# Kernel tuning notes

Measured on AMD Instinct MI355X. Metric: run time of the kernel, lower is better.

Reference implementation:

```python
import jax, jax.numpy as jnp
import numpy as np

N = 50000      # nodes
E = 800000     # edges (avg degree 16)
IN = 16        # input feature dim
H = 512        # hidden dim
L = 3          # num conv layers
G = 256        # graphs per batch
EPS = 1e-5


def setup_inputs() -> dict:
    key = jax.random.key(0)
    ks = jax.random.split(key, 10)
    s = lambda d: 1.0 / np.sqrt(d)
    x = jax.random.normal(ks[0], (N, IN), jnp.float32)
    edge_index = jax.random.randint(ks[1], (2, E), 0, N, dtype=jnp.int64)
    batch = jnp.sort(jax.random.randint(ks[2], (N,), 0, G, dtype=jnp.int64))
    W_in = jax.random.normal(ks[3], (IN, H), jnp.float32) * s(IN)
    b_in = jnp.zeros((H,), jnp.float32)
    W_root = jax.random.normal(ks[4], (L, H, H), jnp.float32) * s(H)
    W_neigh = jax.random.normal(ks[5], (L, H, H), jnp.float32) * s(H)
    b_conv = jnp.zeros((L, H), jnp.float32)
    ln_gamma = jnp.ones((L, H), jnp.float32)
    ln_beta = jnp.zeros((L, H), jnp.float32)
    W_out = jax.random.normal(ks[6], (H, H), jnp.float32) * s(H)
    b_out = jnp.zeros((H,), jnp.float32)
    return {
        'x': x, 'edge_index': edge_index, 'batch': batch,
        'W_in': W_in, 'b_in': b_in,
        'W_root': W_root, 'W_neigh': W_neigh, 'b_conv': b_conv,
        'ln_gamma': ln_gamma, 'ln_beta': ln_beta,
        'W_out': W_out, 'b_out': b_out,
    }


def layer_norm(h, gamma, beta):
    mu = jnp.mean(h, axis=-1, keepdims=True)
    var = jnp.mean((h - mu) ** 2, axis=-1, keepdims=True)
    return (h - mu) * jax.lax.rsqrt(var + EPS) * gamma + beta


def reference(x, edge_index, batch, W_in, b_in, W_root, W_neigh, b_conv,
              ln_gamma, ln_beta, W_out, b_out):
    src, dst = edge_index[0], edge_index[1]
    h = x @ W_in + b_in                                  # [N, H]
    for l in range(L):
        # GraphConv: root transform + sum-aggregated neighbor transform
        agg = jax.ops.segment_sum(h[src], dst, num_segments=N)   # [N, H]
        h = h @ W_root[l] + agg @ W_neigh[l] + b_conv[l]
        h = jax.nn.relu(layer_norm(h, ln_gamma[l], ln_beta[l]))
        # dropout is identity in eval mode
    # mean pool per graph
    pooled = jax.ops.segment_sum(h, batch, num_segments=G)        # [G, H]
    counts = jax.ops.segment_sum(jnp.ones((N, 1), h.dtype), batch, num_segments=G)
    pooled = pooled / jnp.maximum(counts, 1.0)
    return pooled @ W_out + b_out
```

## Files before the change

### kernel.cpp

```cpp
#include <hip/hip_runtime.h>
#include <hip/hip_fp16.h>
#include <stdint.h>

#define N_NODES 50000
#define N_EDGES 800000
#define DIM_IN  16
#define H       512
#define GRAPHS  256
#define AK      1024
#define KT_STEPS 32

typedef __attribute__((ext_vector_type(8))) short short8;
typedef __attribute__((ext_vector_type(8))) _Float16 half8;
typedef __attribute__((ext_vector_type(4))) float f32x4;
typedef __attribute__((ext_vector_type(2))) float f32x2;
typedef __attribute__((ext_vector_type(4))) unsigned int u32x4;
typedef __attribute__((ext_vector_type(2))) unsigned int u32x2;

__device__ __forceinline__ unsigned short f2bf(float f) {
    unsigned int u = __float_as_uint(f);
    return (unsigned short)((u + 0x7fffu + ((u >> 16) & 1u)) >> 16);
}
__device__ __forceinline__ unsigned short f2h(float f) {
    __half h = __float2half(f);
    return *(unsigned short*)&h;
}

#define GLOAD_LDS16(g, l) __builtin_amdgcn_global_load_lds( \
    (const __attribute__((address_space(1))) void*)(g), \
    (__attribute__((address_space(3))) void*)(l), 16, 0, 0)

__global__ void k_count(const int* __restrict__ ei, int* __restrict__ deg) {
    int t = blockIdx.x * 256 + threadIdx.x;
    if (t < N_EDGES) atomicAdd(&deg[ei[N_EDGES + t]], 1);
}

__global__ void k_scan1(const int* __restrict__ deg, int* __restrict__ off, int* __restrict__ bsum) {
    __shared__ int ls[512];
    int t = threadIdx.x; int gi = blockIdx.x * 512 + t;
    ls[t] = (gi < N_NODES) ? deg[gi] : 0;
    __syncthreads();
    for (int o = 1; o < 512; o <<= 1) {
        int u = (t >= o) ? ls[t - o] : 0;
        __syncthreads();
        ls[t] += u;
        __syncthreads();
    }
    if (gi < N_NODES) off[gi] = (t == 0) ? 0 : ls[t - 1];
    if (t == 511) bsum[blockIdx.x] = ls[511];
}

__global__ void k_scan2(int* bsum) {
    __shared__ int ls[128];
    int t = threadIdx.x;
    ls[t] = (t < 98) ? bsum[t] : 0;
    __syncthreads();
    for (int o = 1; o < 128; o <<= 1) {
        int u = (t >= o) ? ls[t - o] : 0;
        __syncthreads();
        ls[t] += u;
        __syncthreads();
    }
    if (t < 98) bsum[t] = (t == 0) ? 0 : ls[t - 1];
}

__global__ void k_scan3(int* __restrict__ off, const int* __restrict__ bsum, int* __restrict__ cur) {
    int i = blockIdx.x * 256 + threadIdx.x;
    if (i < N_NODES) {
        int v = off[i] + bsum[i >> 9];
        off[i] = v; cur[i] = v;
    }
    if (i == 0) off[N_NODES] = N_EDGES;
}

__global__ void k_fill(const int* __restrict__ ei, int* __restrict__ cur, int* __restrict__ csr) {
    int t = blockIdx.x * 256 + threadIdx.x;
    if (t < N_EDGES) {
        int d = ei[N_EDGES + t];
        int p = atomicAdd(&cur[d], 1);
        csr[p] = ei[t];
    }
}

__global__ void k_gemm_in(const float* __restrict__ x, const float* __restrict__ Win,
                          const float* __restrict__ bin, unsigned short* A,
                          unsigned char* __restrict__ h8) {
    __shared__ float Wl[DIM_IN * H];
    __shared__ float xl[16 * DIM_IN];
    __shared__ float bl[H];
    int t = threadIdx.x;
    const float4* W4 = (const float4*)Win;
    float4* Wl4 = (float4*)Wl;
#pragma unroll
    for (int i = 0; i < 8; i++) Wl4[t + 256 * i] = W4[t + 256 * i];
    bl[t] = bin[t]; bl[t + 256] = bin[t + 256];
    int r0 = blockIdx.x * 16;
    {
        int r = t >> 4, k = t & 15;
        int row = r0 + r;
        xl[t] = (row < N_NODES) ? x[row * DIM_IN + k] : 0.f;
    }
    __syncthreads();
    int c0 = t * 2;
    for (int r = 0; r < 16; r++) {
        int row = r0 + r;
        if (row >= N_NODES) break;
        float a0 = bl[c0], a1 = bl[c0 + 1];
#pragma unroll
        for (int k = 0; k < 16; k++) {
            float xv = xl[r * 16 + k];
            a0 += xv * Wl[k * 512 + c0];
            a1 += xv * Wl[k * 512 + c0 + 1];
        }
        unsigned int pack = ((unsigned int)f2bf(a1) << 16) | (unsigned int)f2bf(a0);
        *(unsigned int*)&A[(size_t)row * AK + c0] = pack;
        unsigned int pk8 = (unsigned int)__builtin_amdgcn_cvt_pk_fp8_f32(a0, a1, 0, false);
        *(unsigned short*)&h8[(size_t)row * 512 + c0] = (unsigned short)(pk8 & 0xffffu);
    }
}

__global__ void k_aggregate(const int* __restrict__ off, const int* __restrict__ csr,
                            const unsigned char* __restrict__ h8, unsigned short* A) {
    int w = threadIdx.x >> 6, lane = threadIdx.x & 63;
    int n = blockIdx.x * 4 + w;
    if (n >= N_NODES) return;
    int s = off[n], e = off[n + 1];
    float acc[8] = {0, 0, 0, 0, 0, 0, 0, 0};
    const unsigned char* Ab = h8 + (size_t)lane * 8;

#define ACC_FP8(vv) { \
    f32x2 p0 = __builtin_amdgcn_cvt_pk_f32_fp8((int)(vv)[0], false); \
    f32x2 p1 = __builtin_amdgcn_cvt_pk_f32_fp8((int)(vv)[0], true);  \
    f32x2 p2 = __builtin_amdgcn_cvt_pk_f32_fp8((int)(vv)[1], false); \
    f32x2 p3 = __builtin_amdgcn_cvt_pk_f32_fp8((int)(vv)[1], true);  \
    acc[0] += p0[0]; acc[1] += p0[1]; acc[2] += p1[0]; acc[3] += p1[1]; \
    acc[4] += p2[0]; acc[5] += p2[1]; acc[6] += p3[0]; acc[7] += p3[1]; }

    for (int base = s; base < e; base += 64) {
        int m = e - base; if (m > 64) m = 64;
        int idx = (lane < m) ? csr[base + lane] : 0;
        int g = 0;
        for (; g + 4 <= m; g += 4) {
            int sn0 = __shfl(idx, g);
            int sn1 = __shfl(idx, g + 1);
            int sn2 = __shfl(idx, g + 2);
            int sn3 = __shfl(idx, g + 3);
            u32x2 v0 = *(const u32x2*)(Ab + ((size_t)sn0 << 9));
            u32x2 v1 = *(const u32x2*)(Ab + ((size_t)sn1 << 9));
            u32x2 v2 = *(const u32x2*)(Ab + ((size_t)sn2 << 9));
            u32x2 v3 = *(const u32x2*)(Ab + ((size_t)sn3 << 9));
            ACC_FP8(v0); ACC_FP8(v1); ACC_FP8(v2); ACC_FP8(v3);
        }
        for (; g < m; g++) {
            int sn = __shfl(idx, g);
            u32x2 v = *(const u32x2*)(Ab + ((size_t)sn << 9));
            ACC_FP8(v);
        }
    }
#undef ACC_FP8
    u32x4 hv;
#pragma unroll
    for (int j = 0; j < 4; j++) {
        hv[j] = ((unsigned int)f2h(acc[2 * j + 1]) << 16) | (unsigned int)f2h(acc[2 * j]);
    }
    *(u32x4*)&A[(size_t)n * AK + 512 + lane * 8] = hv;
}

__global__ __launch_bounds__(512, 4)
void k_gemm_layer(unsigned short* A, const unsigned short* __restrict__ Bp,
                  const float* __restrict__ bias, const float* __restrict__ gamma,
                  const float* __restrict__ beta,
                  unsigned char* __restrict__ h8, int w8) {
    extern __shared__ __align__(16) char smem[];
    int t = threadIdx.x, w = t >> 6, lane = t & 63;
    int wr = w >> 1, wc = w & 1;
    int rblk = blockIdx.x * 64;

    f32x4 acc[16];
#pragma unroll
    for (int i = 0; i < 16; i++) acc[i] = (f32x4)(0.f);

    int rowSt = rblk + w * 16 + (lane & 15);
    if (rowSt >= N_NODES) rowSt = N_NODES - 1;
    const unsigned short* gAst = A + (size_t)rowSt * AK + (lane >> 4) * 8;
    const unsigned short* gB = Bp + (size_t)lane * 8;

    auto STAGE = [&](int kt, int buf) {
        char* base = smem + buf * 36864;
        const unsigned short* gBk = gB + (size_t)kt * 32 * 512;
#pragma unroll
        for (int i = 0; i < 4; i++) {
            int cf = w * 4 + i;
            GLOAD_LDS16(gBk + (size_t)cf * 512, base + cf * 1024);
        }
        if (w < 4) GLOAD_LDS16(gAst + kt * 32, base + 32768 + w * 1024);
    };

    STAGE(0, 0);
    __syncthreads();

    for (int kt = 0; kt < 16; kt++) {
        int cur = kt & 1;
        STAGE(kt + 1, cur ^ 1);
        char* base = smem + cur * 36864;
        short8 av = *(const short8*)(base + 32768 + wr * 1024 + lane * 16);
#pragma unroll
        for (int i = 0; i < 16; i++) {
            short8 bv = *(const short8*)(base + (wc * 16 + i) * 1024 + lane * 16);
            acc[i] = __builtin_amdgcn_mfma_f32_16x16x32_bf16(av, bv, acc[i], 0, 0, 0);
        }
        __syncthreads();
    }
    for (int kt = 16; kt < 32; kt++) {
        int cur = kt & 1;
        if (kt + 1 < 32) STAGE(kt + 1, cur ^ 1);
        char* base = smem + cur * 36864;
        half8 av = *(const half8*)(base + 32768 + wr * 1024 + lane * 16);
#pragma unroll
        for (int i = 0; i < 16; i++) {
            half8 bv = *(const half8*)(base + (wc * 16 + i) * 1024 + lane * 16);
            acc[i] = __builtin_amdgcn_mfma_f32_16x16x32_f16(av, bv, acc[i], 0, 0, 0);
        }
        __syncthreads();
    }

    int g = lane >> 4, cl = lane & 15;
    float s[4] = {0, 0, 0, 0}, q[4] = {0, 0, 0, 0};
#pragma unroll
    for (int i = 0; i < 16; i++) {
        int col = wc * 256 + i * 16 + cl;
        float b = bias[col];
        f32x4 a = acc[i];
#pragma unroll
        for (int r = 0; r < 4; r++) {
            float v = a[r] + b;
            a[r] = v;
            s[r] += v;
            q[r] += v * v;
        }
        acc[i] = a;
    }
#pragma unroll
    for (int m = 1; m < 16; m <<= 1) {
#pragma unroll
        for (int r = 0; r < 4; r++) {
            s[r] += __shfl_xor(s[r], m);
            q[r] += __shfl_xor(q[r], m);
        }
    }
    float* pbuf = (float*)smem;
    if (cl == 0) {
#pragma unroll
        for (int r = 0; r < 4; r++) {
            pbuf[((wr * 2 + wc) * 16) + g * 4 + r] = s[r];
            pbuf[256 + ((wr * 2 + wc) * 16) + g * 4 + r] = q[r];
        }
    }
    __syncthreads();
    float mean[4], rs[4];
#pragma unroll
    for (int r = 0; r < 4; r++) {
        float sf = pbuf[(wr * 2) * 16 + g * 4 + r] + pbuf[(wr * 2 + 1) * 16 + g * 4 + r];
        float qf = pbuf[256 + (wr * 2) * 16 + g * 4 + r] + pbuf[256 + (wr * 2 + 1) * 16 + g * 4 + r];
        mean[r] = sf * (1.f / 512.f);
        float var = qf * (1.f / 512.f) - mean[r] * mean[r];
        rs[r] = rsqrtf(var + 1e-5f);
    }
    int row0 = rblk + wr * 16 + g * 4;
    bool ok[4];
#pragma unroll
    for (int r = 0; r < 4; r++) ok[r] = (row0 + r) < N_NODES;
#pragma unroll
    for (int i = 0; i < 16; i++) {
        int col = wc * 256 + i * 16 + cl;
        float ga = gamma[col], be = beta[col];
        f32x4 a = acc[i];
#pragma unroll
        for (int r = 0; r < 4; r++) {
            float o = (a[r] - mean[r]) * rs[r] * ga + be;
            o = fmaxf(o, 0.f);
            if (ok[r]) {
                A[(size_t)(row0 + r) * AK + col] = f2bf(o);
                if (w8) {
                    unsigned int pk8 = (unsigned int)__builtin_amdgcn_cvt_pk_fp8_f32(o, o, 0, false);
                    h8[(size_t)(row0 + r) * 512 + col] = (unsigned char)(pk8 & 0xffu);
                }
            }
        }
    }
}

__global__ void k_pool(const unsigned short* __restrict__ A, const int* __restrict__ batch,
                       float* __restrict__ pooled) {
    __shared__ float part[4 * 512];
    __shared__ int se[2];
    int g = blockIdx.x, t = threadIdx.x, w = t >> 6, lane = t & 63;
    if (t == 0) {
        int lo = 0, hi = N_NODES;
        while (lo < hi) { int m = (lo + hi) >> 1; if (batch[m] < g) lo = m + 1; else hi = m; }
        se[0] = lo;
        int lo2 = lo; hi = N_NODES;
        while (lo2 < hi) { int m = (lo2 + hi) >> 1; if (batch[m] < g + 1) lo2 = m + 1; else hi = m; }
        se[1] = lo2;
    }
    __syncthreads();
    int s = se[0], e = se[1];
    float acc[8] = {0, 0, 0, 0, 0, 0, 0, 0};
    for (int row = s + w; row < e; row += 4) {
        u32x4 v = *(const u32x4*)&A[(size_t)row * AK + lane * 8];
#pragma unroll
        for (int j = 0; j < 4; j++) {
            unsigned int uu = v[j];
            acc[2 * j]     += __uint_as_float(uu << 16);
            acc[2 * j + 1] += __uint_as_float(uu & 0xffff0000u);
        }
    }
#pragma unroll
    for (int j = 0; j < 8; j++) part[w * 512 + j * 64 + lane] = acc[j];
    __syncthreads();
    float cnt = fmaxf((float)(e - s), 1.f);
    for (int sidx = t; sidx < 512; sidx += 256) {
        float v = part[sidx] + part[512 + sidx] + part[1024 + sidx] + part[1536 + sidx];
        int col = (sidx & 63) * 8 + (sidx >> 6);
        pooled[(size_t)g * 512 + col] = v / cnt;
    }
}

__global__ __launch_bounds__(256)
void k_out(const float* __restrict__ pooled, const float* __restrict__ Wout,
           const float* __restrict__ bout, float* __restrict__ out) {
    __shared__ float pl[8 * 512];
    int t = threadIdx.x;
    int g0 = blockIdx.x * 8;
#pragma unroll
    for (int i = 0; i < 16; i++) {
        int idx = i * 256 + t;
        pl[idx] = pooled[(size_t)g0 * 512 + idx];
    }
    __syncthreads();
    int c0 = t * 2;
    float a[8][2];
#pragma unroll
    for (int g = 0; g < 8; g++) { a[g][0] = bout[c0]; a[g][1] = bout[c0 + 1]; }
    for (int k = 0; k < 512; k++) {
        float2 wv = *(const float2*)&Wout[(size_t)k * 512 + c0];
#pragma unroll
        for (int g = 0; g < 8; g++) {
            float p = pl[g * 512 + k];
            a[g][0] += p * wv.x;
            a[g][1] += p * wv.y;
        }
    }
#pragma unroll
    for (int g = 0; g < 8; g++) {
        out[(size_t)(g0 + g) * 512 + c0]     = a[g][0];
        out[(size_t)(g0 + g) * 512 + c0 + 1] = a[g][1];
    }
}

__global__ void k_pack_b(const float* __restrict__ Wr, const float* __restrict__ Wn,
                         unsigned short* __restrict__ Bp) {
    int t = blockIdx.x * 256 + threadIdx.x;
    if (t >= 3 * KT_STEPS * 32 * 64) return;
    int lane = t & 63;
    int u = t >> 6;
    int cf = u & 31; u >>= 5;
    int kt = u % KT_STEPS;
    int l  = u / KT_STEPS;
    int col = cf * 16 + (lane & 15);
    int kr0 = (kt & 15) * 32 + (lane >> 4) * 8;
    bool isRoot = (kt < 16);
    const float* W = (isRoot ? Wr : Wn) + (size_t)l * H * H;
    unsigned int words[4];
#pragma unroll
    for (int p = 0; p < 4; p++) {
        float v0 = W[(size_t)(kr0 + 2 * p) * H + col];
        float v1 = W[(size_t)(kr0 + 2 * p + 1) * H + col];
        unsigned short b0 = isRoot ? f2bf(v0) : f2h(v0);
        unsigned short b1 = isRoot ? f2bf(v1) : f2h(v1);
        words[p] = ((unsigned int)b1 << 16) | (unsigned int)b0;
    }
    u32x4 v; v[0] = words[0]; v[1] = words[1]; v[2] = words[2]; v[3] = words[3];
    *(u32x4*)&Bp[(size_t)t * 8] = v;
}

extern "C" void kernel_launch(void* const* d_in, const int* in_sizes, int n_in,
                              void* d_out, int out_size, void* d_ws, size_t ws_size,
                              hipStream_t stream) {
    const float* x     = (const float*)d_in[0];
    const int*   ei    = (const int*)d_in[1];
    const int*   batch = (const int*)d_in[2];
    const float* Win   = (const float*)d_in[3];
    const float* bin   = (const float*)d_in[4];
    const float* Wr    = (const float*)d_in[5];
    const float* Wn    = (const float*)d_in[6];
    const float* bconv = (const float*)d_in[7];
    const float* gamma = (const float*)d_in[8];
    const float* beta  = (const float*)d_in[9];
    const float* Wout  = (const float*)d_in[10];
    const float* bout  = (const float*)d_in[11];
    float* out = (float*)d_out;

    char* p = (char*)d_ws;
    auto carve = [&](size_t bytes) { char* r = p; p += (bytes + 255) & ~(size_t)255; return r; };
    unsigned short* A  = (unsigned short*)carve((size_t)N_NODES * AK * 2);
    unsigned char*  h8 = (unsigned char*)carve((size_t)N_NODES * 512);
    unsigned short* Bp = (unsigned short*)carve((size_t)3 * KT_STEPS * 32 * 64 * 8 * 2);
    int* csr  = (int*)carve((size_t)N_EDGES * 4);
    int* deg  = (int*)carve((size_t)N_NODES * 4);
    int* off  = (int*)carve((size_t)(N_NODES + 1) * 4);
    int* cur  = (int*)carve((size_t)N_NODES * 4);
    int* bsum = (int*)carve(1024);
    float* pooled = (float*)carve((size_t)GRAPHS * H * 4);

    hipMemsetAsync(deg, 0, (size_t)N_NODES * 4, stream);
    k_count<<<(N_EDGES + 255) / 256, 256, 0, stream>>>(ei, deg);
    k_scan1<<<98, 512, 0, stream>>>(deg, off, bsum);
    k_scan2<<<1, 128, 0, stream>>>(bsum);
    k_scan3<<<(N_NODES + 255) / 256, 256, 0, stream>>>(off, bsum, cur);
    k_fill<<<(N_EDGES + 255) / 256, 256, 0, stream>>>(ei, cur, csr);
    k_gemm_in<<<(N_NODES + 15) / 16, 256, 0, stream>>>(x, Win, bin, A, h8);
    k_pack_b<<<(3 * KT_STEPS * 32 * 64) / 256, 256, 0, stream>>>(Wr, Wn, Bp);
    for (int l = 0; l < 3; l++) {
        k_aggregate<<<(N_NODES + 3) / 4, 256, 0, stream>>>(off, csr, h8, A);
        k_gemm_layer<<<(N_NODES + 63) / 64, 512, 73728, stream>>>(
            A, Bp + (size_t)l * KT_STEPS * 32 * 64 * 8,
            bconv + (size_t)l * H, gamma + (size_t)l * H, beta + (size_t)l * H,
            h8, (l < 2) ? 1 : 0);
    }
    k_pool<<<GRAPHS, 256, 0, stream>>>(A, batch, pooled);
    k_out<<<32, 256, 0, stream>>>(pooled, Wout, bout, out);
}
```

Before: 662.9 us.

## Use FP8 root GEMM with ping-pong FP8 activations and coalesced epilogue stores

The root-transform half of the layer GEMM now reads the FP8 activation copy directly and uses fp8×fp8 MFMA with FP8-packed root weights, instead of a separate bf16 copy of h. A operands are loaded straight into registers and prefetched one step ahead rather than staged in LDS. The interleaved A buffer is split into separate agg and ping-pong h8 buffers. The epilogue writes FP8 outputs through shared memory so the global stores are coalesced, and only the last layer writes bf16. This cuts memory traffic and bf16 stores, at the cost of lower precision in the root GEMM (FP8 weights and activations).

```diff
diff --git a/kernel.cpp b/kernel.cpp
--- a/kernel.cpp
+++ b/kernel.cpp
@@ -7,8 +7,6 @@
 #define DIM_IN  16
 #define H       512
 #define GRAPHS  256
-#define AK      1024
-#define KT_STEPS 32
 
 typedef __attribute__((ext_vector_type(8))) short short8;
 typedef __attribute__((ext_vector_type(8))) _Float16 half8;
@@ -83,8 +81,7 @@
 }
 
 __global__ void k_gemm_in(const float* __restrict__ x, const float* __restrict__ Win,
-                          const float* __restrict__ bin, unsigned short* A,
-                          unsigned char* __restrict__ h8) {
+                          const float* __restrict__ bin, unsigned char* __restrict__ h8) {
     __shared__ float Wl[DIM_IN * H];
     __shared__ float xl[16 * DIM_IN];
     __shared__ float bl[H];
@@ -112,15 +109,13 @@
             a0 += xv * Wl[k * 512 + c0];
             a1 += xv * Wl[k * 512 + c0 + 1];
         }
-        unsigned int pack = ((unsigned int)f2bf(a1) << 16) | (unsigned int)f2bf(a0);
-        *(unsigned int*)&A[(size_t)row * AK + c0] = pack;
         unsigned int pk8 = (unsigned int)__builtin_amdgcn_cvt_pk_fp8_f32(a0, a1, 0, false);
         *(unsigned short*)&h8[(size_t)row * 512 + c0] = (unsigned short)(pk8 & 0xffffu);
     }
 }
 
 __global__ void k_aggregate(const int* __restrict__ off, const int* __restrict__ csr,
-                            const unsigned char* __restrict__ h8, unsigned short* A) {
+                            const unsigned char* __restrict__ h8, unsigned short* __restrict__ agg) {
     int w = threadIdx.x >> 6, lane = threadIdx.x & 63;
     int n = blockIdx.x * 4 + w;
     if (n >= N_NODES) return;
@@ -163,14 +158,15 @@
     for (int j = 0; j < 4; j++) {
         hv[j] = ((unsigned int)f2h(acc[2 * j + 1]) << 16) | (unsigned int)f2h(acc[2 * j]);
     }
-    *(u32x4*)&A[(size_t)n * AK + 512 + lane * 8] = hv;
+    *(u32x4*)&agg[(size_t)n * 512 + lane * 8] = hv;
 }
 
 __global__ __launch_bounds__(512, 4)
-void k_gemm_layer(unsigned short* A, const unsigned short* __restrict__ Bp,
+void k_gemm_layer(const unsigned char* __restrict__ h8in, const unsigned short* __restrict__ agg,
+                  unsigned char* __restrict__ h8out, unsigned short* __restrict__ hout,
+                  const unsigned char* __restrict__ Bp8, const unsigned short* __restrict__ Bpf,
                   const float* __restrict__ bias, const float* __restrict__ gamma,
-                  const float* __restrict__ beta,
-                  unsigned char* __restrict__ h8, int w8) {
+                  const float* __restrict__ beta, int lastLayer) {
     extern __shared__ __align__(16) char smem[];
     int t = threadIdx.x, w = t >> 6, lane = t & 63;
     int wr = w >> 1, wc = w & 1;
@@ -180,48 +176,57 @@
 #pragma unroll
     for (int i = 0; i < 16; i++) acc[i] = (f32x4)(0.f);
 
-    int rowSt = rblk + w * 16 + (lane & 15);
-    if (rowSt >= N_NODES) rowSt = N_NODES - 1;
-    const unsigned short* gAst = A + (size_t)rowSt * AK + (lane >> 4) * 8;
-    const unsigned short* gB = Bp + (size_t)lane * 8;
-
-    auto STAGE = [&](int kt, int buf) {
-        char* base = smem + buf * 36864;
-        const unsigned short* gBk = gB + (size_t)kt * 32 * 512;
+    int rowA = rblk + wr * 16 + (lane & 15);
+    if (rowA >= N_NODES) rowA = N_NODES - 1;
+    const unsigned char* aRow8 = h8in + (size_t)rowA * 512 + (lane >> 4) * 8;
+    const unsigned char* aRowF = (const unsigned char*)agg + (size_t)rowA * 1024 + (lane >> 4) * 16;
+    const unsigned char* BpfB = (const unsigned char*)Bpf;
+
+    auto STAGE8 = [&](int kt, int buf) {
+        const unsigned char* g = Bp8 + (size_t)kt * 16384 + w * 2048 + lane * 16;
+        char* base = smem + buf * 32768 + w * 2048;
+        GLOAD_LDS16(g, base);
+        GLOAD_LDS16(g + 1024, base + 1024);
+    };
+    auto STAGEF = [&](int ktf, int buf) {
+        const unsigned char* g = BpfB + (size_t)ktf * 32768 + lane * 16;
+        char* base = smem + buf * 32768;
 #pragma unroll
         for (int i = 0; i < 4; i++) {
             int cf = w * 4 + i;
-            GLOAD_LDS16(gBk + (size_t)cf * 512, base + cf * 1024);
-        }
-        if (w < 4) GLOAD_LDS16(gAst + kt * 32, base + 32768 + w * 1024);
+            GLOAD_LDS16(g + cf * 1024, base + cf * 1024);
+        }
     };
 
-    STAGE(0, 0);
-    __syncthreads();
-
-    for (int kt = 0; kt < 16; kt++) {
+    long a8c = *(const long*)(aRow8);
+    long a8n = 0;
+    half8 a16c = (half8)(_Float16)0, a16n = (half8)(_Float16)0;
+    STAGE8(0, 0);
+    __syncthreads();
+
+    for (int kt = 0; kt < 32; kt++) {
         int cur = kt & 1;
-        STAGE(kt + 1, cur ^ 1);
-        char* base = smem + cur * 36864;
-        short8 av = *(const short8*)(base + 32768 + wr * 1024 + lane * 16);
-#pragma unroll
-        for (int i = 0; i < 16; i++) {
-            short8 bv = *(const short8*)(base + (wc * 16 + i) * 1024 + lane * 16);
-            acc[i] = __builtin_amdgcn_mfma_f32_16x16x32_bf16(av, bv, acc[i], 0, 0, 0);
-        }
-        __syncthreads();
-    }
-    for (int kt = 16; kt < 32; kt++) {
-        int cur = kt & 1;
-        if (kt + 1 < 32) STAGE(kt + 1, cur ^ 1);
-        char* base = smem + cur * 36864;
-        half8 av = *(const half8*)(base + 32768 + wr * 1024 + lane * 16);
-#pragma unroll
-        for (int i = 0; i < 16; i++) {
-            half8 bv = *(const half8*)(base + (wc * 16 + i) * 1024 + lane * 16);
-            acc[i] = __builtin_amdgcn_mfma_f32_16x16x32_f16(av, bv, acc[i], 0, 0, 0);
-        }
-        __syncthreads();
+        if (kt < 15)       a8n  = *(const long*)(aRow8 + (kt + 1) * 32);
+        else if (kt < 31)  a16n = *(const half8*)(aRowF + (kt - 15) * 64);
+        if (kt < 15)       STAGE8(kt + 1, cur ^ 1);
+        else if (kt < 31)  STAGEF(kt - 15, cur ^ 1);
+        char* base = smem + cur * 32768;
+        if (kt < 16) {
+#pragma unroll
+            for (int i = 0; i < 16; i++) {
+                long bv = *(const long*)(base + (wc * 16 + i) * 512 + lane * 8);
+                acc[i] = __builtin_amdgcn_mfma_f32_16x16x32_fp8_fp8(a8c, bv, acc[i], 0, 0, 0);
+            }
+        } else {
+#pragma unroll
+            for (int i = 0; i < 16; i++) {
+                half8 bv = *(const half8*)(base + (wc * 16 + i) * 1024 + lane * 16);
+                acc[i] = __builtin_amdgcn_mfma_f32_16x16x32_f16(a16c, bv, acc[i], 0, 0, 0);
+            }
+        }
+        __syncthreads();
+        a8c = a8n;
+        a16c = a16n;
     }
 
     int g = lane >> 4, cl = lane & 15;
@@ -266,31 +271,53 @@
         float var = qf * (1.f / 512.f) - mean[r] * mean[r];
         rs[r] = rsqrtf(var + 1e-5f);
     }
+    __syncthreads();
     int row0 = rblk + wr * 16 + g * 4;
-    bool ok[4];
-#pragma unroll
-    for (int r = 0; r < 4; r++) ok[r] = (row0 + r) < N_NODES;
-#pragma unroll
-    for (int i = 0; i < 16; i++) {
-        int col = wc * 256 + i * 16 + cl;
-        float ga = gamma[col], be = beta[col];
-        f32x4 a = acc[i];
-#pragma unroll
-        for (int r = 0; r < 4; r++) {
-            float o = (a[r] - mean[r]) * rs[r] * ga + be;
-            o = fmaxf(o, 0.f);
-            if (ok[r]) {
-                A[(size_t)(row0 + r) * AK + col] = f2bf(o);
-                if (w8) {
-                    unsigned int pk8 = (unsigned int)__builtin_amdgcn_cvt_pk_fp8_f32(o, o, 0, false);
-                    h8[(size_t)(row0 + r) * 512 + col] = (unsigned char)(pk8 & 0xffu);
-                }
+    if (lastLayer) {
+        bool ok[4];
+#pragma unroll
+        for (int r = 0; r < 4; r++) ok[r] = (row0 + r) < N_NODES;
+#pragma unroll
+        for (int i = 0; i < 16; i++) {
+            int col = wc * 256 + i * 16 + cl;
+            float ga = gamma[col], be = beta[col];
+            f32x4 a = acc[i];
+#pragma unroll
+            for (int r = 0; r < 4; r++) {
+                float o = (a[r] - mean[r]) * rs[r] * ga + be;
+                o = fmaxf(o, 0.f);
+                if (ok[r]) hout[(size_t)(row0 + r) * 512 + col] = f2bf(o);
             }
         }
-    }
-}
-
-__global__ void k_pool(const unsigned short* __restrict__ A, const int* __restrict__ batch,
+    } else {
+#pragma unroll
+        for (int i = 0; i < 16; i++) {
+            int col = wc * 256 + i * 16 + cl;
+            float ga = gamma[col], be = beta[col];
+            f32x4 a = acc[i];
+#pragma unroll
+            for (int r = 0; r < 4; r++) {
+                float o = (a[r] - mean[r]) * rs[r] * ga + be;
+                o = fmaxf(o, 0.f);
+                unsigned int pk8 = (unsigned int)__builtin_amdgcn_cvt_pk_fp8_f32(o, o, 0, false);
+                smem[(wr * 16 + g * 4 + r) * 512 + col] = (char)(pk8 & 0xffu);
+            }
+        }
+        __syncthreads();
+        int row = t >> 3, off = (t & 7) * 64;
+        if (rblk + row < N_NODES) {
+            unsigned char* dst = h8out + (size_t)(rblk + row) * 512 + off;
+            const char* src = smem + row * 512 + off;
+#pragma unroll
+            for (int j = 0; j < 4; j++) {
+                u32x4 v = *(const u32x4*)(src + j * 16);
+                *(u32x4*)(dst + j * 16) = v;
+            }
+        }
+    }
+}
+
+__global__ void k_pool(const unsigned short* __restrict__ hbf, const int* __restrict__ batch,
                        float* __restrict__ pooled) {
     __shared__ float part[4 * 512];
     __shared__ int se[2];
@@ -307,7 +334,7 @@
     int s = se[0], e = se[1];
     float acc[8] = {0, 0, 0, 0, 0, 0, 0, 0};
     for (int row = s + w; row < e; row += 4) {
-        u32x4 v = *(const u32x4*)&A[(size_t)row * AK + lane * 8];
+        u32x4 v = *(const u32x4*)&hbf[(size_t)row * 512 + lane * 8];
 #pragma unroll
         for (int j = 0; j < 4; j++) {
             unsigned int uu = v[j];
@@ -359,29 +386,42 @@
 }
 
 __global__ void k_pack_b(const float* __restrict__ Wr, const float* __restrict__ Wn,
-                         unsigned short* __restrict__ Bp) {
-    int t = blockIdx.x * 256 + threadIdx.x;
-    if (t >= 3 * KT_STEPS * 32 * 64) return;
+                         unsigned char* __restrict__ Bp8, unsigned short* __restrict__ Bpf) {
+    int tid = blockIdx.x * 256 + threadIdx.x;
+    const int HALF = 3 * 16 * 32 * 64;
+    if (tid >= 2 * HALF) return;
+    bool isRoot = (tid < HALF);
+    int t = isRoot ? tid : tid - HALF;
     int lane = t & 63;
     int u = t >> 6;
     int cf = u & 31; u >>= 5;
-    int kt = u % KT_STEPS;
-    int l  = u / KT_STEPS;
+    int kt = u & 15;
+    int l  = u >> 4;
     int col = cf * 16 + (lane & 15);
-    int kr0 = (kt & 15) * 32 + (lane >> 4) * 8;
-    bool isRoot = (kt < 16);
-    const float* W = (isRoot ? Wr : Wn) + (size_t)l * H * H;
-    unsigned int words[4];
-#pragma unroll
-    for (int p = 0; p < 4; p++) {
-        float v0 = W[(size_t)(kr0 + 2 * p) * H + col];
-        float v1 = W[(size_t)(kr0 + 2 * p + 1) * H + col];
-        unsigned short b0 = isRoot ? f2bf(v0) : f2h(v0);
-        unsigned short b1 = isRoot ? f2bf(v1) : f2h(v1);
-        words[p] = ((unsigned int)b1 << 16) | (unsigned int)b0;
-    }
-    u32x4 v; v[0] = words[0]; v[1] = words[1]; v[2] = words[2]; v[3] = words[3];
-    *(u32x4*)&Bp[(size_t)t * 8] = v;
+    int kr0 = kt * 32 + (lane >> 4) * 8;
+    if (isRoot) {
+        const float* W = Wr + (size_t)l * H * H;
+        float v[8];
+#pragma unroll
+        for (int j = 0; j < 8; j++) v[j] = W[(size_t)(kr0 + j) * H + col];
+        int w0 = __builtin_amdgcn_cvt_pk_fp8_f32(v[0], v[1], 0, false);
+        w0 = __builtin_amdgcn_cvt_pk_fp8_f32(v[2], v[3], w0, true);
+        int w1 = __builtin_amdgcn_cvt_pk_fp8_f32(v[4], v[5], 0, false);
+        w1 = __builtin_amdgcn_cvt_pk_fp8_f32(v[6], v[7], w1, true);
+        u32x2 o; o[0] = (unsigned int)w0; o[1] = (unsigned int)w1;
+        *(u32x2*)&Bp8[(size_t)((l * 16 + kt) * 32 + cf) * 512 + lane * 8] = o;
+    } else {
+        const float* W = Wn + (size_t)l * H * H;
+        unsigned int words[4];
+#pragma unroll
+        for (int p = 0; p < 4; p++) {
+            float v0 = W[(size_t)(kr0 + 2 * p) * H + col];
+            float v1 = W[(size_t)(kr0 + 2 * p + 1) * H + col];
+            words[p] = ((unsigned int)f2h(v1) << 16) | (unsigned int)f2h(v0);
+        }
+        u32x4 v; v[0] = words[0]; v[1] = words[1]; v[2] = words[2]; v[3] = words[3];
+        *(u32x4*)&Bpf[(size_t)((l * 16 + kt) * 32 + cf) * 512 + lane * 8] = v;
+    }
 }
 
 extern "C" void kernel_launch(void* const* d_in, const int* in_sizes, int n_in,
@@ -403,9 +443,12 @@
 
     char* p = (char*)d_ws;
     auto carve = [&](size_t bytes) { char* r = p; p += (bytes + 255) & ~(size_t)255; return r; };
-    unsigned short* A  = (unsigned short*)carve((size_t)N_NODES * AK * 2);
-    unsigned char*  h8 = (unsigned char*)carve((size_t)N_NODES * 512);
-    unsigned short* Bp = (unsigned short*)carve((size_t)3 * KT_STEPS * 32 * 64 * 8 * 2);
+    unsigned char*  h8a  = (unsigned char*)carve((size_t)N_NODES * 512);
+    unsigned char*  h8b  = (unsigned char*)carve((size_t)N_NODES * 512);
+    unsigned short* agg  = (unsigned short*)carve((size_t)N_NODES * 512 * 2);
+    unsigned short* hout = (unsigned short*)carve((size_t)N_NODES * 512 * 2);
+    unsigned char*  Bp8  = (unsigned char*)carve((size_t)3 * 16 * 32 * 64 * 8);
+    unsigned short* Bpf  = (unsigned short*)carve((size_t)3 * 16 * 32 * 64 * 8 * 2);
     int* csr  = (int*)carve((size_t)N_EDGES * 4);
     int* deg  = (int*)carve((size_t)N_NODES * 4);
     int* off  = (int*)carve((size_t)(N_NODES + 1) * 4);
@@ -419,15 +462,20 @@
     k_scan2<<<1, 128, 0, stream>>>(bsum);
     k_scan3<<<(N_NODES + 255) / 256, 256, 0, stream>>>(off, bsum, cur);
     k_fill<<<(N_EDGES + 255) / 256, 256, 0, stream>>>(ei, cur, csr);
-    k_gemm_in<<<(N_NODES + 15) / 16, 256, 0, stream>>>(x, Win, bin, A, h8);
-    k_pack_b<<<(3 * KT_STEPS * 32 * 64) / 256, 256, 0, stream>>>(Wr, Wn, Bp);
+    k_gemm_in<<<(N_NODES + 15) / 16, 256, 0, stream>>>(x, Win, bin, h8a);
+    k_pack_b<<<(2 * 3 * 16 * 32 * 64 + 255) / 256, 256, 0, stream>>>(Wr, Wn, Bp8, Bpf);
+
+    unsigned char* hcur = h8a;
+    unsigned char* hnxt = h8b;
     for (int l = 0; l < 3; l++) {
-        k_aggregate<<<(N_NODES + 3) / 4, 256, 0, stream>>>(off, csr, h8, A);
-        k_gemm_layer<<<(N_NODES + 63) / 64, 512, 73728, stream>>>(
-            A, Bp + (size_t)l * KT_STEPS * 32 * 64 * 8,
+        k_aggregate<<<(N_NODES + 3) / 4, 256, 0, stream>>>(off, csr, hcur, agg);
+        k_gemm_layer<<<(N_NODES + 63) / 64, 512, 65536, stream>>>(
+            hcur, agg, hnxt, hout,
+            Bp8 + (size_t)l * 16 * 16384, Bpf + (size_t)l * 16 * 16384,
             bconv + (size_t)l * H, gamma + (size_t)l * H, beta + (size_t)l * H,
-            h8, (l < 2) ? 1 : 0);
-    }
-    k_pool<<<GRAPHS, 256, 0, stream>>>(A, batch, pooled);
+            (l == 2) ? 1 : 0);
+        unsigned char* tmp = hcur; hcur = hnxt; hnxt = tmp;
+    }
+    k_pool<<<GRAPHS, 256, 0, stream>>>(hout, batch, pooled);
     k_out<<<32, 256, 0, stream>>>(pooled, Wout, bout, out);
 }
```

Result: faster. 623.1 us (-6.0%).
